# Kernel optimization log

Measured on AMD Instinct MI355X. Metric: run time of the kernel, lower is better.

The kernel has to match this reference:

```python
import jax, jax.numpy as jnp
import numpy as np
from jax.scipy.linalg import expm

NUM_QUBITS = 10
D = 2 ** NUM_QUBITS  # 1024
B, S = 8, 4096


def setup_inputs() -> dict:
    key = jax.random.key(0)
    k_x, k_mr, k_mi = jax.random.split(key, 3)
    inputs = jax.random.normal(k_x, (B, S, D), dtype=jnp.float32)
    M_real = 0.1 * jax.random.normal(k_mr, (D, D), dtype=jnp.float32)
    M_imag = 0.1 * jax.random.normal(k_mi, (D, D), dtype=jnp.float32)
    bias = jnp.zeros((D,), dtype=jnp.float32)
    qubit_gate = jnp.ones((D,), dtype=jnp.float32)
    return {"inputs": inputs, "M_real": M_real, "M_imag": M_imag,
            "bias": bias, "qubit_gate": qubit_gate}


def _l2_normalize(x, axis=-1, eps=1e-12):
    # matches tf.linalg.l2_normalize: x * rsqrt(max(sum(x^2), eps))
    ss = jnp.sum(jnp.square(x), axis=axis, keepdims=True)
    return x * jax.lax.rsqrt(jnp.maximum(ss, eps))


def reference(inputs, M_real, M_imag, bias, qubit_gate):
    norm_inputs = _l2_normalize(inputs, axis=-1)
    A = M_real - M_real.T  # skew-symmetric -> expm(A) is orthogonal
    Bm = M_imag - M_imag.T
    U = expm(A) @ expm(Bm)  # [D, D]
    transformed = jnp.einsum('bsd,de->bse', norm_inputs, U) + bias
    measured = jnp.square(transformed)
    gate_probs = jax.nn.softmax(qubit_gate)  # [D]
    gated_output = measured * gate_probs
    return gated_output, gate_probs
```

## Files before the change

### kernel.cpp

```cpp
#include <hip/hip_runtime.h>


typedef unsigned int u32;
typedef unsigned short u16;
typedef __attribute__((ext_vector_type(8))) short short8;
typedef __attribute__((ext_vector_type(4))) float f32x4;

#define GLOBAL_AS __attribute__((address_space(1)))
#define LDS_AS    __attribute__((address_space(3)))

constexpr int D = 1024;
constexpr float EXPM_SCALE = 1.0f / 8.0f;

__device__ __forceinline__ u16 f2bf(float f) {
  union { float f; u32 u; } v; v.f = f;
  u32 r = (v.u + 0x7FFFu + ((v.u >> 16) & 1u)) >> 16;
  return (u16)r;
}
__device__ __forceinline__ float bf2f(u16 u) {
  union { u32 u; float f; } v; v.u = ((u32)u) << 16;
  return v.f;
}

__device__ __forceinline__ void g2l16(const void* g, void* l) {
  __builtin_amdgcn_global_load_lds((const GLOBAL_AS u32*)g, (LDS_AS u32*)l,
                                   16, 0, 0);
}

#define WAITV(N)                                                   \
  do {                                                             \
    asm volatile("s_waitcnt vmcnt(" #N ")" ::: "memory");          \
    __builtin_amdgcn_sched_barrier(0);                             \
  } while (0)

__device__ void norm_rows8(const float* __restrict__ x, u16* __restrict__ Xn,
                           int r0, int tid, float* sred) {
  float4 v[8];
#pragma unroll
  for (int i = 0; i < 8; ++i)
    v[i] = ((const float4*)(x + (size_t)(r0 + i) * D))[tid];
  float ss[8];
#pragma unroll
  for (int i = 0; i < 8; ++i)
    ss[i] = v[i].x * v[i].x + v[i].y * v[i].y + v[i].z * v[i].z +
            v[i].w * v[i].w;
  for (int o = 32; o; o >>= 1)
#pragma unroll
    for (int i = 0; i < 8; ++i) ss[i] += __shfl_down(ss[i], o);
  const int w = tid >> 6;
  if ((tid & 63) == 0)
#pragma unroll
    for (int i = 0; i < 8; ++i) sred[i * 4 + w] = ss[i];
  __syncthreads();
#pragma unroll
  for (int i = 0; i < 8; ++i) {
    const float tot =
        sred[i * 4 + 0] + sred[i * 4 + 1] + sred[i * 4 + 2] + sred[i * 4 + 3];
    const float inv = rsqrtf(fmaxf(tot, 1e-12f));
    ushort4 o4;
    o4.x = f2bf(v[i].x * inv); o4.y = f2bf(v[i].y * inv);
    o4.z = f2bf(v[i].z * inv); o4.w = f2bf(v[i].w * inv);
    ((ushort4*)(Xn + (size_t)(r0 + i) * D))[tid] = o4;
  }
}

struct SkewParams {
  const float *Mr, *Mi;
  u16 *X0, *X1;
  const float* x;
  u16* Xn;
  int row0;
};
__global__ __launch_bounds__(256) void skew_norm_kernel(SkewParams p) {
  __shared__ __align__(16) float t2[64][67];
  const int bid = blockIdx.x, tid = threadIdx.x;
  if (bid >= 512) {
    norm_rows8(p.x, p.Xn, p.row0 + (bid - 512) * 8, tid, &t2[0][0]);
    return;
  }
  const int z = bid >> 8, t = bid & 255;
  const float* M = z ? p.Mi : p.Mr;
  u16* X = z ? p.X1 : p.X0;
  const int bi = t >> 4, bj = t & 15;
  const int r0 = tid >> 4, c0 = (tid & 15) * 4;
  float4 own[4];
#pragma unroll
  for (int i = 0; i < 4; ++i) {
    const int r = i * 16 + r0;
    own[i] = *(const float4*)(M + (size_t)(bi * 64 + r) * D + bj * 64 + c0);
    const float4 tr =
        *(const float4*)(M + (size_t)(bj * 64 + r) * D + bi * 64 + c0);
    t2[r][c0 + 0] = tr.x; t2[r][c0 + 1] = tr.y;
    t2[r][c0 + 2] = tr.z; t2[r][c0 + 3] = tr.w;
  }
  __syncthreads();
#pragma unroll
  for (int i = 0; i < 4; ++i) {
    const int r = i * 16 + r0;
    const float o[4] = {own[i].x, own[i].y, own[i].z, own[i].w};
    ushort4 hv;
    u16* hp = (u16*)&hv;
#pragma unroll
    for (int j = 0; j < 4; ++j)
      hp[j] = f2bf((o[j] - t2[c0 + j][r]) * EXPM_SCALE);
    *(ushort4*)(X + (size_t)(bi * 64 + r) * D + bj * 64 + c0) = hv;
  }
}

struct CJob {
  const u16 *A, *B;
  const float* C;
  u16 *Dst, *DT;
  float alpha;
};
struct GNParams {
  CJob jobs[2];
  int njobs;
  const float* x;
  u16* Xn;
  int row0;
};
__global__ __launch_bounds__(256) void gemm_norm_kernel(GNParams p) {
  __shared__ __align__(16) u16 ldsA[3][4096];
  __shared__ __align__(16) u16 ldsB[3][4096];
  const int bid = blockIdx.x, tid = threadIdx.x;
  if (bid >= p.njobs) {
    norm_rows8(p.x, p.Xn, p.row0 + (bid - p.njobs) * 8, tid,
               (float*)&ldsA[0][0]);
    return;
  }
  const CJob jb = p.jobs[bid >> 8];
  const int bi = (bid >> 4) & 15, bj = bid & 15;
  const int w = tid >> 6, lane = tid & 63;
  const int wr = w >> 1, wc = w & 1;
  f32x4 acc[2][2];
#pragma unroll
  for (int m = 0; m < 2; ++m)
#pragma unroll
    for (int n = 0; n < 2; ++n) acc[m][n] = f32x4{0.f, 0.f, 0.f, 0.f};
  const int r_l = lane >> 3, c_l = lane & 7;

  auto stage = [&](int buf, int kt) {
    const int k0 = kt * 64;
#pragma unroll
    for (int pp = 0; pp < 2; ++pp) {
      const int row = pp * 32 + w * 8 + r_l;
      const int chunk = c_l ^ (row & 7);
      g2l16(jb.A + (size_t)(bi * 64 + row) * D + k0 + chunk * 8,
            (char*)&ldsA[buf][0] + pp * 4096 + w * 1024);
      g2l16(jb.B + (size_t)(bj * 64 + row) * D + k0 + chunk * 8,
            (char*)&ldsB[buf][0] + pp * 4096 + w * 1024);
    }
  };
  auto compute = [&](int buf) {
#pragma unroll
    for (int h = 0; h < 2; ++h) {
      const int kk = h * 32 + (lane >> 4) * 8;
      short8 a[2], b[2];
#pragma unroll
      for (int m = 0; m < 2; ++m) {
        const int row = wr * 32 + m * 16 + (lane & 15);
        const int off = row * 128 + ((kk * 2) ^ ((row & 7) << 4));
        a[m] = *(const short8*)((const char*)&ldsA[buf][0] + off);
      }
#pragma unroll
      for (int n = 0; n < 2; ++n) {
        const int row = wc * 32 + n * 16 + (lane & 15);
        const int off = row * 128 + ((kk * 2) ^ ((row & 7) << 4));
        b[n] = *(const short8*)((const char*)&ldsB[buf][0] + off);
      }
#pragma unroll
      for (int m = 0; m < 2; ++m)
#pragma unroll
        for (int n = 0; n < 2; ++n)
          acc[m][n] = __builtin_amdgcn_mfma_f32_16x16x32_bf16(
              a[m], b[n], acc[m][n], 0, 0, 0);
    }
  };

  stage(0, 0); stage(1, 1);
  for (int s = 0; s < 14; ++s) {
    WAITV(4);
    __builtin_amdgcn_s_barrier();
    __builtin_amdgcn_sched_barrier(0);
    stage((s + 2) % 3, s + 2);
    compute(s % 3);
  }
  WAITV(4);
  __builtin_amdgcn_s_barrier();
  __builtin_amdgcn_sched_barrier(0);
  compute(14 % 3);
  WAITV(0);
  __builtin_amdgcn_s_barrier();
  __builtin_amdgcn_sched_barrier(0);
  compute(15 % 3);

  const int or0 = bi * 64 + wr * 32, oc0 = bj * 64 + wc * 32;
#pragma unroll
  for (int m = 0; m < 2; ++m)
#pragma unroll
    for (int n = 0; n < 2; ++n) {
      const int row0 = or0 + m * 16 + (lane >> 4) * 4;
      const int col = oc0 + n * 16 + (lane & 15);
      ushort4 dv;
      u16* dp = (u16*)&dv;
#pragma unroll
      for (int r = 0; r < 4; ++r) {
        float v = acc[m][n][r] * jb.alpha;
        if (jb.C) v += jb.C[(size_t)(row0 + r) * D + col];
        dp[r] = f2bf(v);
        jb.Dst[(size_t)(row0 + r) * D + col] = dp[r];
      }
      if (jb.DT)
        *(ushort4*)(jb.DT + (size_t)col * D + row0) = dv;
    }
}

struct X34Params {
  const u16 *X[2], *X2[2];
  u16 *X3[2], *X4[2], *q1t[2];
  float* q0[2];
  const float* qg;
  float* gate_out;
  const float* x;
  u16* Xn;
  int row0;
};
__global__ __launch_bounds__(256) void x34q_norm_kernel(X34Params p) {
  __shared__ __align__(16) u16 ldsA[3][2048];
  __shared__ __align__(16) u16 ldsB1[3][2048];
  __shared__ __align__(16) u16 ldsB2[3][2048];
  const int bid = blockIdx.x, tid = threadIdx.x;
  if (bid > 512) {
    norm_rows8(p.x, p.Xn, p.row0 + (bid - 513) * 8, tid, (float*)&ldsA[0][0]);
    return;
  }
  if (bid == 512) {
    float* red = (float*)&ldsA[0][0];
    const float4 v = ((const float4*)p.qg)[tid];
    float mx = fmaxf(fmaxf(v.x, v.y), fmaxf(v.z, v.w));
    for (int o = 32; o; o >>= 1) mx = fmaxf(mx, __shfl_xor(mx, o));
    if ((tid & 63) == 0) red[tid >> 6] = mx;
    __syncthreads();
    const float M = fmaxf(fmaxf(red[0], red[1]), fmaxf(red[2], red[3]));
    __syncthreads();
    const float e0 = __expf(v.x - M), e1 = __expf(v.y - M),
                e2 = __expf(v.z - M), e3 = __expf(v.w - M);
    float s = e0 + e1 + e2 + e3;
    for (int o = 32; o; o >>= 1) s += __shfl_xor(s, o);
    if ((tid & 63) == 0) red[tid >> 6] = s;
    __syncthreads();
    const float S = red[0] + red[1] + red[2] + red[3];
    const float4 o4 = {e0 / S, e1 / S, e2 / S, e3 / S};
    ((float4*)p.gate_out)[tid] = o4;
    return;
  }
  const int mz = bid >> 8, t = bid & 255;
  const int bi = t >> 4, bj = t & 15;
  const u16* Ag = p.X2[mz];
  const u16* B1g = p.X[mz];
  const u16* B2g = p.X2[mz];
  const int w = tid >> 6, lane = tid & 63;
  const int wr = w >> 1, wc = w & 1;
  f32x4 acc3[2][2], acc4[2][2];
#pragma unroll
  for (int m = 0; m < 2; ++m)
#pragma unroll
    for (int n = 0; n < 2; ++n) {
      acc3[m][n] = f32x4{0.f, 0.f, 0.f, 0.f};
      acc4[m][n] = f32x4{0.f, 0.f, 0.f, 0.f};
    }
  const int srow = tid >> 2, sc = tid & 3;

  auto stage = [&](int buf, int s) {
    const int k0 = s * 32;
    const int csrc = sc ^ (srow & 3);
    g2l16(Ag + (size_t)(bi * 64 + srow) * D + k0 + csrc * 8,
          (char*)&ldsA[buf][0] + tid * 16);
    g2l16(B1g + (size_t)(bj * 64 + srow) * D + k0 + csrc * 8,
          (char*)&ldsB1[buf][0] + tid * 16);
    g2l16(B2g + (size_t)(bj * 64 + srow) * D + k0 + csrc * 8,
          (char*)&ldsB2[buf][0] + tid * 16);
  };
  const int h4 = lane >> 4;
  auto compute = [&](int buf) {
    short8 a[2], b1[2], b2[2];
#pragma unroll
    for (int m = 0; m < 2; ++m) {
      const int row = wr * 32 + m * 16 + (lane & 15);
      const int off = row * 64 + ((h4 ^ (row & 3)) << 4);
      a[m] = *(const short8*)((const char*)&ldsA[buf][0] + off);
    }
#pragma unroll
    for (int n = 0; n < 2; ++n) {
      const int row = wc * 32 + n * 16 + (lane & 15);
      const int off = row * 64 + ((h4 ^ (row & 3)) << 4);
      b1[n] = *(const short8*)((const char*)&ldsB1[buf][0] + off);
      b2[n] = *(const short8*)((const char*)&ldsB2[buf][0] + off);
    }
#pragma unroll
    for (int m = 0; m < 2; ++m)
#pragma unroll
      for (int n = 0; n < 2; ++n) {
        acc3[m][n] = __builtin_amdgcn_mfma_f32_16x16x32_bf16(
            a[m], b1[n], acc3[m][n], 0, 0, 0);
        acc4[m][n] = __builtin_amdgcn_mfma_f32_16x16x32_bf16(
            a[m], b2[n], acc4[m][n], 0, 0, 0);
      }
  };

  stage(0, 0); stage(1, 1);
  for (int s = 0; s < 30; ++s) {
    WAITV(3);
    __builtin_amdgcn_s_barrier();
    __builtin_amdgcn_sched_barrier(0);
    stage((s + 2) % 3, s + 2);
    compute(s % 3);
  }
  WAITV(3);
  __builtin_amdgcn_s_barrier();
  __builtin_amdgcn_sched_barrier(0);
  compute(30 % 3);
  WAITV(0);
  __builtin_amdgcn_s_barrier();
  __builtin_amdgcn_sched_barrier(0);
  compute(31 % 3);

  const int or0 = bi * 64 + wr * 32, oc0 = bj * 64 + wc * 32;
#pragma unroll
  for (int m = 0; m < 2; ++m)
#pragma unroll
    for (int n = 0; n < 2; ++n) {
      const int row0 = or0 + m * 16 + (lane >> 4) * 4;
      const int col = oc0 + n * 16 + (lane & 15);
#pragma unroll
      for (int r = 0; r < 4; ++r) {
        const size_t idx = (size_t)(row0 + r) * D + col;
        const u16 x3v = f2bf(-acc3[m][n][r]);
        const u16 x4v = f2bf(acc4[m][n][r]);
        p.X3[mz][idx] = x3v;
        p.X4[mz][idx] = x4v;
        const float d = (row0 + r == col) ? 1.f : 0.f;
        const float xf = bf2f(p.X[mz][idx]);
        const float x2f = bf2f(p.X2[mz][idx]);
        const float x3f = bf2f(x3v), x4f = bf2f(x4v);
        p.q0[mz][idx] = d + xf + x2f * 0.5f + x3f * (1.f / 6.f);
        p.q1t[mz][idx] =
            f2bf(d * (1.f / 24.f) - xf * (1.f / 120.f) + x2f * (1.f / 720.f) -
                 x3f * (1.f / 5040.f) + x4f * (1.f / 40320.f));
      }
    }
}

__global__ __launch_bounds__(512, 1) void main_gemm_kernel(
    const u16* __restrict__ Xn, const u16* __restrict__ Wm,
    const float* __restrict__ bias, const float* __restrict__ gate,
    float* __restrict__ out) {
  const int tid = threadIdx.x;
  const int wid = tid >> 6, lane = tid & 63;
  const int wr = wid >> 2, wc = wid & 3;
  __shared__ u16 lds[4 * 16384];
  f32x4 acc[8][4];
#pragma unroll
  for (int m = 0; m < 8; ++m)
#pragma unroll
    for (int n = 0; n < 4; ++n) acc[m][n] = f32x4{0.f, 0.f, 0.f, 0.f};

  const int bi = blockIdx.x, bj = blockIdx.y;
  const int r_ = tid >> 2;
  const int c_ = tid & 3;

  auto stage = [&](int s) {
    char* base = (char*)lds + (s & 3) * 32768;
#pragma unroll
    for (int pp = 0; pp < 2; ++pp) {
      const int row = pp * 128 + r_;
      const int csrc = c_ ^ ((row >> 1) & 3);
      g2l16(Xn + (size_t)(bi * 256 + row) * D + s * 32 + csrc * 8,
            base + pp * 8192 + tid * 16);
      g2l16(Wm + (size_t)(bj * 256 + row) * D + s * 32 + csrc * 8,
            base + 16384 + pp * 8192 + tid * 16);
    }
  };

  const int h = lane >> 4;
  auto compute = [&](int s) {
    const char* base = (const char*)lds + (s & 3) * 32768;
    short8 a[8], b[4];
#pragma unroll
    for (int m = 0; m < 8; ++m) {
      const int row = wr * 128 + m * 16 + (lane & 15);
      const int off = row * 64 + ((h ^ ((row >> 1) & 3)) << 4);
      a[m] = *(const short8*)(base + off);
    }
#pragma unroll
    for (int n = 0; n < 4; ++n) {
      const int row = wc * 64 + n * 16 + (lane & 15);
      const int off = 16384 + row * 64 + ((h ^ ((row >> 1) & 3)) << 4);
      b[n] = *(const short8*)(base + off);
    }
    __builtin_amdgcn_s_setprio(1);
#pragma unroll
    for (int m = 0; m < 8; ++m)
#pragma unroll
      for (int n = 0; n < 4; ++n)
        acc[m][n] = __builtin_amdgcn_mfma_f32_16x16x32_bf16(a[m], b[n],
                                                            acc[m][n], 0, 0, 0);
    __builtin_amdgcn_s_setprio(0);
  };

  stage(0); stage(1); stage(2);
  for (int s = 0; s < 29; ++s) {
    WAITV(8);
    __builtin_amdgcn_s_barrier();
    __builtin_amdgcn_sched_barrier(0);
    stage(s + 3);
    compute(s);
  }
  WAITV(8);
  __builtin_amdgcn_s_barrier();
  __builtin_amdgcn_sched_barrier(0);
  compute(29);
  WAITV(4);
  __builtin_amdgcn_s_barrier();
  __builtin_amdgcn_sched_barrier(0);
  compute(30);
  WAITV(0);
  __builtin_amdgcn_s_barrier();
  __builtin_amdgcn_sched_barrier(0);
  compute(31);

  const int or0 = bi * 256 + wr * 128, oc0 = bj * 256 + wc * 64;
#pragma unroll
  for (int m = 0; m < 8; ++m)
#pragma unroll
    for (int n = 0; n < 4; ++n) {
      const int col = oc0 + n * 16 + (lane & 15);
      const float bc = bias[col], gc = gate[col];
#pragma unroll
      for (int r = 0; r < 4; ++r) {
        const int row = or0 + m * 16 + (lane >> 4) * 4 + r;
        const float t = acc[m][n][r] + bc;
        out[(size_t)row * D + col] = t * t * gc;
      }
    }
}

extern "C" void kernel_launch(void* const* d_in, const int* in_sizes, int n_in,
                              void* d_out, int out_size, void* d_ws,
                              size_t ws_size, hipStream_t stream) {
  (void)in_sizes; (void)n_in; (void)out_size; (void)ws_size;
  const float* inp = (const float*)d_in[0];
  const float* Mr = (const float*)d_in[1];
  const float* Mi = (const float*)d_in[2];
  const float* bias = (const float*)d_in[3];
  const float* qg = (const float*)d_in[4];
  float* out = (float*)d_out;
  float* gate_out = out + (size_t)32768 * 1024;

  char* ws = (char*)d_ws;
  u16* Xn = (u16*)ws;
  auto slot = [&](int m, int s) -> u16* {
    return (u16*)(ws + 67108864 + (size_t)m * 16777216 + (size_t)s * 2097152);
  };
  auto q0p = [&](int m) -> float* {
    return (float*)(ws + 67108864 + (size_t)m * 16777216 + 12582912);
  };
  u16* W = (u16*)(ws + 100663296);

  const int CH = 4096, NB = 512;
  int row0 = 0;

  {
    SkewParams sp{Mr, Mi, slot(0, 0), slot(1, 0), inp, Xn, row0};
    skew_norm_kernel<<<512 + NB, 256, 0, stream>>>(sp);
    row0 += CH;
  }
  GNParams gp{};
  gp.x = inp; gp.Xn = Xn;
  for (int m = 0; m < 2; ++m)
    gp.jobs[m] = CJob{slot(m, 0), slot(m, 0), nullptr, slot(m, 1), nullptr,
                      -1.f};
  gp.njobs = 512; gp.row0 = row0;
  gemm_norm_kernel<<<512 + NB, 256, 0, stream>>>(gp);
  row0 += CH;
  {
    X34Params xp{};
    for (int m = 0; m < 2; ++m) {
      xp.X[m] = slot(m, 0); xp.X2[m] = slot(m, 1);
      xp.X3[m] = slot(m, 2); xp.X4[m] = slot(m, 3);
      xp.q1t[m] = slot(m, 4); xp.q0[m] = q0p(m);
    }
    xp.qg = qg; xp.gate_out = gate_out;
    xp.x = inp; xp.Xn = Xn; xp.row0 = row0;
    x34q_norm_kernel<<<513 + NB, 256, 0, stream>>>(xp);
    row0 += CH;
  }
  for (int m = 0; m < 2; ++m)
    gp.jobs[m] = CJob{slot(m, 3), slot(m, 4), q0p(m), slot(m, 0), slot(m, 1),
                      1.f};
  gp.njobs = 512; gp.row0 = row0;
  gemm_norm_kernel<<<512 + NB, 256, 0, stream>>>(gp);
  row0 += CH;
  for (int m = 0; m < 2; ++m)
    gp.jobs[m] = CJob{slot(m, 0), slot(m, 1), nullptr, slot(m, 2), slot(m, 4),
                      1.f};
  gp.row0 = row0;
  gemm_norm_kernel<<<512 + NB, 256, 0, stream>>>(gp);
  row0 += CH;
  for (int m = 0; m < 2; ++m)
    gp.jobs[m] = CJob{slot(m, 2), slot(m, 4), nullptr, slot(m, 3), slot(m, 5),
                      1.f};
  gp.row0 = row0;
  gemm_norm_kernel<<<512 + NB, 256, 0, stream>>>(gp);
  row0 += CH;
  for (int m = 0; m < 2; ++m)
    gp.jobs[m] = CJob{slot(m, 3), slot(m, 5), nullptr, slot(m, 0), slot(m, 1),
                      1.f};
  gp.row0 = row0;
  gemm_norm_kernel<<<512 + NB, 256, 0, stream>>>(gp);
  row0 += CH;
  gp.jobs[0] = CJob{slot(1, 1), slot(0, 0), nullptr, W, nullptr, 1.f};
  gp.njobs = 256; gp.row0 = row0;
  gemm_norm_kernel<<<256 + NB, 256, 0, stream>>>(gp);

  main_gemm_kernel<<<dim3(128, 4), 512, 0, stream>>>(Xn, W, bias, gate_out,
                                                     out);
}
```

Measured before the change: 217.7 us.

## Use one fewer expm squaring step and redistribute normalization rows across stages

Changes the expm scaling from 1/8 to 1/4, so one repeated-squaring GEMM stage is dropped and the final product reads different slots. The input-normalization rows that were overlapped with each matrix stage are rebalanced into larger chunks to cover all rows with one fewer launch. This removes a full D×D GEMM launch. The cost is a larger scaled norm for the Taylor/Padé step, which may reduce expm accuracy.

New measurement: 207.5 us. -4.7%, faster.

```diff
diff --git a/kernel.cpp b/kernel.cpp
--- a/kernel.cpp
+++ b/kernel.cpp
@@ -10,7 +10,7 @@
 #define LDS_AS    __attribute__((address_space(3)))
 
 constexpr int D = 1024;
-constexpr float EXPM_SCALE = 1.0f / 8.0f;
+constexpr float EXPM_SCALE = 1.0f / 4.0f;
 
 __device__ __forceinline__ u16 f2bf(float f) {
   union { float f; u32 u; } v; v.f = f;
@@ -468,13 +468,12 @@
   };
   u16* W = (u16*)(ws + 100663296);
 
-  const int CH = 4096, NB = 512;
   int row0 = 0;
 
   {
     SkewParams sp{Mr, Mi, slot(0, 0), slot(1, 0), inp, Xn, row0};
-    skew_norm_kernel<<<512 + NB, 256, 0, stream>>>(sp);
-    row0 += CH;
+    skew_norm_kernel<<<512 + 585, 256, 0, stream>>>(sp);
+    row0 += 4680;
   }
   GNParams gp{};
   gp.x = inp; gp.Xn = Xn;
@@ -482,8 +481,8 @@
     gp.jobs[m] = CJob{slot(m, 0), slot(m, 0), nullptr, slot(m, 1), nullptr,
                       -1.f};
   gp.njobs = 512; gp.row0 = row0;
-  gemm_norm_kernel<<<512 + NB, 256, 0, stream>>>(gp);
-  row0 += CH;
+  gemm_norm_kernel<<<512 + 585, 256, 0, stream>>>(gp);
+  row0 += 4680;
   {
     X34Params xp{};
     for (int m = 0; m < 2; ++m) {
@@ -493,36 +492,30 @@
     }
     xp.qg = qg; xp.gate_out = gate_out;
     xp.x = inp; xp.Xn = Xn; xp.row0 = row0;
-    x34q_norm_kernel<<<513 + NB, 256, 0, stream>>>(xp);
-    row0 += CH;
+    x34q_norm_kernel<<<513 + 585, 256, 0, stream>>>(xp);
+    row0 += 4680;
   }
   for (int m = 0; m < 2; ++m)
     gp.jobs[m] = CJob{slot(m, 3), slot(m, 4), q0p(m), slot(m, 0), slot(m, 1),
                       1.f};
   gp.njobs = 512; gp.row0 = row0;
-  gemm_norm_kernel<<<512 + NB, 256, 0, stream>>>(gp);
-  row0 += CH;
+  gemm_norm_kernel<<<512 + 585, 256, 0, stream>>>(gp);
+  row0 += 4680;
   for (int m = 0; m < 2; ++m)
     gp.jobs[m] = CJob{slot(m, 0), slot(m, 1), nullptr, slot(m, 2), slot(m, 4),
                       1.f};
   gp.row0 = row0;
-  gemm_norm_kernel<<<512 + NB, 256, 0, stream>>>(gp);
-  row0 += CH;
+  gemm_norm_kernel<<<512 + 585, 256, 0, stream>>>(gp);
+  row0 += 4680;
   for (int m = 0; m < 2; ++m)
     gp.jobs[m] = CJob{slot(m, 2), slot(m, 4), nullptr, slot(m, 3), slot(m, 5),
                       1.f};
   gp.row0 = row0;
-  gemm_norm_kernel<<<512 + NB, 256, 0, stream>>>(gp);
-  row0 += CH;
-  for (int m = 0; m < 2; ++m)
-    gp.jobs[m] = CJob{slot(m, 3), slot(m, 5), nullptr, slot(m, 0), slot(m, 1),
-                      1.f};
-  gp.row0 = row0;
-  gemm_norm_kernel<<<512 + NB, 256, 0, stream>>>(gp);
-  row0 += CH;
-  gp.jobs[0] = CJob{slot(1, 1), slot(0, 0), nullptr, W, nullptr, 1.f};
+  gemm_norm_kernel<<<512 + 585, 256, 0, stream>>>(gp);
+  row0 += 4680;
+  gp.jobs[0] = CJob{slot(1, 5), slot(0, 3), nullptr, W, nullptr, 1.f};
   gp.njobs = 256; gp.row0 = row0;
-  gemm_norm_kernel<<<256 + NB, 256, 0, stream>>>(gp);
+  gemm_norm_kernel<<<256 + 586, 256, 0, stream>>>(gp);
 
   main_gemm_kernel<<<dim3(128, 4), 512, 0, stream>>>(Xn, W, bias, gate_out,
                                                      out);
```
